# Performance work log

Hardware: AMD Instinct MI355X
Metric: run time of the kernel (lower is better)

Reference implementation:

```python
import jax, jax.numpy as jnp
import numpy as np

EPS = 1e-5
N_HEAD = 16


def layernorm(x, g, b):
    mu = jnp.mean(x, axis=-1, keepdims=True)
    var = jnp.mean(jnp.square(x - mu), axis=-1, keepdims=True)
    return (x - mu) * jax.lax.rsqrt(var + EPS) * g + b


def setup_inputs() -> dict:
    key = jax.random.key(0)
    ks = jax.random.split(key, 8)
    B, S, D = 4, 2048, 1024
    F = 4 * D
    s = 0.02
    return {
        "h": jax.random.normal(ks[0], (B, S, D), jnp.float32),
        "ln1_g": jnp.ones((D,), jnp.float32),
        "ln1_b": jnp.zeros((D,), jnp.float32),
        "wq": jax.random.normal(ks[1], (D, D), jnp.float32) * s,
        "bq": jnp.zeros((D,), jnp.float32),
        "wk": jax.random.normal(ks[2], (D, D), jnp.float32) * s,
        "bk": jnp.zeros((D,), jnp.float32),
        "wv": jax.random.normal(ks[3], (D, D), jnp.float32) * s,
        "bv": jnp.zeros((D,), jnp.float32),
        "wo": jax.random.normal(ks[4], (D, D), jnp.float32) * s,
        "bo": jnp.zeros((D,), jnp.float32),
        "ln2_g": jnp.ones((D,), jnp.float32),
        "ln2_b": jnp.zeros((D,), jnp.float32),
        "wfc": jax.random.normal(ks[5], (F, D), jnp.float32) * s,
        "bfc": jnp.zeros((F,), jnp.float32),
        "wproj": jax.random.normal(ks[6], (D, F), jnp.float32) * s,
        "bproj": jnp.zeros((D,), jnp.float32),
    }


def reference(h, ln1_g, ln1_b, wq, bq, wk, bk, wv, bv, wo, bo,
              ln2_g, ln2_b, wfc, bfc, wproj, bproj):
    B, S, D = h.shape
    H = N_HEAD
    Dh = D // H

    # --- attention sub-block ---
    r = h
    x = layernorm(h, ln1_g, ln1_b)
    q = (x @ wq.T + bq).reshape(B, S, H, Dh)
    k = (x @ wk.T + bk).reshape(B, S, H, Dh)
    v = (x @ wv.T + bv).reshape(B, S, H, Dh)

    scores = jnp.einsum("bqhd,bkhd->bhqk", q, k) / jnp.sqrt(jnp.float32(Dh))
    causal = jnp.tril(jnp.ones((S, S), bool))  # [S,S]
    scores = jnp.where(causal, scores, jnp.finfo(scores.dtype).min)
    probs = jax.nn.softmax(scores, axis=-1)
    o = jnp.einsum("bhqk,bkhd->bqhd", probs, v).reshape(B, S, D)
    h = r + (o @ wo.T + bo)

    # --- MLP sub-block ---
    r = h
    x = layernorm(h, ln2_g, ln2_b)
    x = jax.nn.gelu(x @ wfc.T + bfc, approximate=True)  # NewGELU (tanh)
    h = r + (x @ wproj.T + bproj)
    return h
```

## Files before the change

### kernel.cpp

```cpp
#include <hip/hip_runtime.h>
#include <hip/hip_bf16.h>
#include <stdint.h>


typedef short bf16x8 __attribute__((ext_vector_type(8)));
typedef float f32x4  __attribute__((ext_vector_type(4)));
typedef float f32x16 __attribute__((ext_vector_type(16)));
typedef short s16x4  __attribute__((ext_vector_type(4)));

__device__ __forceinline__ short f2bf(float f) {
  union { float f; uint32_t u; } a;
  a.f = f;
  uint32_t r = a.u + 0x7fffu + ((a.u >> 16) & 1u);
  return (short)(r >> 16);
}

__device__ __forceinline__ unsigned cvt_pk_bf16(float lo, float hi_) {
  unsigned r;
  asm("v_cvt_pk_bf16_f32 %0, %1, %2" : "=v"(r) : "v"(lo), "v"(hi_));
  return r;
}

__device__ __forceinline__ void gload_lds16(const void* g, void* l) {
  __builtin_amdgcn_global_load_lds(
      (const __attribute__((address_space(1))) void*)g,
      (__attribute__((address_space(3))) void*)l, 16, 0, 0);
}

__device__ __forceinline__ float gelu_f(float x) {
  float y = 0.7978845608028654f * (x + 0.044715f * x * x * x);
  y = fminf(fmaxf(y, -20.f), 20.f);
  float e = __expf(2.f * y);
  return 0.5f * x * (1.f + (e - 1.f) / (e + 1.f));
}

struct W6 {
  const float* s[6];
  short* d[6];
  int off[7];
};

__global__ __launch_bounds__(256)
void cvt_all(W6 a) {
  const int i = blockIdx.x * 256 + threadIdx.x;
#pragma unroll
  for (int k = 0; k < 6; ++k) {
    if (i >= a.off[k] && i < a.off[k + 1]) {
      const int j = i - a.off[k];
      float4 v = ((const float4*)a.s[k])[j];
      s16x4 o;
      o[0] = f2bf(v.x); o[1] = f2bf(v.y); o[2] = f2bf(v.z); o[3] = f2bf(v.w);
      ((s16x4*)a.d[k])[j] = o;
    }
  }
}

__global__ __launch_bounds__(256)
void ln_fwd(const float* __restrict__ x, const float* __restrict__ g,
            const float* __restrict__ b, short* __restrict__ y) {
  const long row = blockIdx.x;
  const int t = threadIdx.x;
  const float4 xv = ((const float4*)(x + row * 1024))[t];
  float s  = xv.x + xv.y + xv.z + xv.w;
  float ss = xv.x * xv.x + xv.y * xv.y + xv.z * xv.z + xv.w * xv.w;
#pragma unroll
  for (int m = 1; m < 64; m <<= 1) {
    s  += __shfl_xor(s, m);
    ss += __shfl_xor(ss, m);
  }
  __shared__ float rs[4], rss[4];
  const int wid = t >> 6, lane = t & 63;
  if (lane == 0) { rs[wid] = s; rss[wid] = ss; }
  __syncthreads();
  s  = rs[0] + rs[1] + rs[2] + rs[3];
  ss = rss[0] + rss[1] + rss[2] + rss[3];
  const float mu   = s * (1.f / 1024.f);
  const float var  = ss * (1.f / 1024.f) - mu * mu;
  const float rstd = rsqrtf(var + 1e-5f);
  const float4 gv = ((const float4*)g)[t];
  const float4 bv = ((const float4*)b)[t];
  s16x4 ov;
  ov[0] = f2bf((xv.x - mu) * rstd * gv.x + bv.x);
  ov[1] = f2bf((xv.y - mu) * rstd * gv.y + bv.y);
  ov[2] = f2bf((xv.z - mu) * rstd * gv.z + bv.z);
  ov[3] = f2bf((xv.w - mu) * rstd * gv.w + bv.w);
  *(s16x4*)(y + row * 1024 + t * 4) = ov;
}

template <int OUT_BF16, int HAS_RES, int HAS_GELU>
__global__ __launch_bounds__(256, 2)
void gemm_bt5(const short* __restrict__ A, const short* __restrict__ W,
              const float* __restrict__ bias, const float* __restrict__ res,
              void* __restrict__ out, int M, int N, int K) {
  __shared__ short As[128 * 64];
  __shared__ short Bs[256 * 64];
  const int tid = threadIdx.x;
  const int wid = tid >> 6, lane = tid & 63;
  const int l16 = lane & 15, lg = lane >> 4;
  const int wm = wid >> 1, wn = wid & 1;

  const int nbx = N >> 8;
  const int nwg = nbx * (M >> 7);
  int flat = (int)blockIdx.x;
  if ((nwg & 7) == 0) flat = (flat & 7) * (nwg >> 3) + (flat >> 3);
  const int brow = (flat / nbx) * 128, bcol = (flat % nbx) * 256;

  f32x4 acc[4][8] = {};

  const int r0 = tid >> 3, g0 = tid & 7;

  int ra[4], rb[8];
#pragma unroll
  for (int m = 0; m < 4; ++m) ra[m] = wm * 64 + m * 16 + l16;
#pragma unroll
  for (int n = 0; n < 8; ++n) rb[n] = wn * 128 + n * 16 + l16;

  for (int kt = 0; kt < K; kt += 64) {
    __syncthreads();
#pragma unroll
    for (int i = 0; i < 4; ++i) {
      const int row = i * 32 + r0;
      gload_lds16(A + (long)(brow + row) * K + kt + 8 * (g0 ^ (row & 7)),
                  &As[(i * 256 + tid) * 8]);
    }
#pragma unroll
    for (int i = 0; i < 8; ++i) {
      const int row = i * 32 + r0;
      gload_lds16(W + (long)(bcol + row) * K + kt + 8 * (g0 ^ (row & 7)),
                  &Bs[(i * 256 + tid) * 8]);
    }
    __syncthreads();

#pragma unroll
    for (int kk = 0; kk < 2; ++kk) {
      bf16x8 af[4], bf[8];
#pragma unroll
      for (int m = 0; m < 4; ++m)
        af[m] = *(const bf16x8*)&As[ra[m] * 64 + 8 * ((kk * 4 + lg) ^ (ra[m] & 7))];
#pragma unroll
      for (int n = 0; n < 8; ++n)
        bf[n] = *(const bf16x8*)&Bs[rb[n] * 64 + 8 * ((kk * 4 + lg) ^ (rb[n] & 7))];
#pragma unroll
      for (int m = 0; m < 4; ++m)
#pragma unroll
        for (int n = 0; n < 8; ++n)
          acc[m][n] = __builtin_amdgcn_mfma_f32_16x16x32_bf16(af[m], bf[n], acc[m][n], 0, 0, 0);
    }
  }

#pragma unroll
  for (int n = 0; n < 8; ++n) {
    const int col = bcol + wn * 128 + n * 16 + l16;
    const float bb = bias[col];
#pragma unroll
    for (int m = 0; m < 4; ++m) {
#pragma unroll
      for (int j = 0; j < 4; ++j) {
        const long row = brow + wm * 64 + m * 16 + lg * 4 + j;
        float vv = acc[m][n][j] + bb;
        if (HAS_GELU) vv = gelu_f(vv);
        if (HAS_RES) vv += res[row * N + col];
        if (OUT_BF16) ((short*)out)[row * N + col] = f2bf(vv);
        else          ((float*)out)[row * N + col] = vv;
      }
    }
  }
}

__global__ __launch_bounds__(256)
void transpose_v(const short* __restrict__ v, short* __restrict__ vtg,
                 int S, int ldv, int H) {
  __shared__ short t[64][66];
  const int bh = blockIdx.y, b = bh / H, hh = bh % H;
  const int s0 = blockIdx.x * 64;
  const int tid = threadIdx.x;
#pragma unroll
  for (int i = 0; i < 2; ++i) {
    const int c = i * 256 + tid;
    const int sl = c >> 3, d8 = (c & 7) * 8;
    bf16x8 vv = *(const bf16x8*)&v[((long)b * S + s0 + sl) * ldv + hh * 64 + d8];
#pragma unroll
    for (int j = 0; j < 8; ++j) t[d8 + j][sl] = vv[j];
  }
  __syncthreads();
#pragma unroll
  for (int i = 0; i < 2; ++i) {
    const int c = i * 256 + tid;
    const int dl = c >> 3, s8 = (c & 7) * 8;
    bf16x8 ov;
#pragma unroll
    for (int j = 0; j < 8; ++j) ov[j] = t[dl][s8 + j];
    *(bf16x8*)&vtg[((long)bh * 64 + dl) * S + s0 + s8] = ov;
  }
}

__global__ __launch_bounds__(256, 4)
void attn_fwd2(const short* __restrict__ qg, const short* __restrict__ kg,
               const short* __restrict__ vtg, short* __restrict__ og,
               int S, int ldq, int D, int H) {
  const int tid = threadIdx.x, wid = tid >> 6, lane = tid & 63;
  const int l31 = lane & 31, hi = lane >> 5;
  const int fid = blockIdx.x;
  const int bh = fid & 63;
  const int b = bh / H, hh = bh % H;
  static const int perm[16] = {15, 0, 8, 7, 1, 14, 6, 9, 13, 2, 10, 5, 3, 12, 4, 11};
  const int qt = perm[(fid >> 6) & 15];
  const int q0 = qt * 128;
  const long qbase = (long)b * S * ldq + hh * 64;
  const long obase = (long)b * S * D + hh * 64;
  const long vbase = (long)bh * 64 * S;

  __shared__ short Ks[2][64 * 64];
  __shared__ short Vs[2][64 * 64];

  auto STAGE = [&](int buf, int k0) {
#pragma unroll
    for (int i = 0; i < 2; ++i) {
      const int c = i * 256 + tid;
      const int row = c >> 3, gl = c & 7;
      gload_lds16(&kg[qbase + (long)(k0 + row) * ldq + 8 * (gl ^ (row & 7))],
                  &Ks[buf][(i * 256 + wid * 64) * 8]);
      gload_lds16(&vtg[vbase + (long)row * S + k0 + 8 * (gl ^ (row & 7))],
                  &Vs[buf][(i * 256 + wid * 64) * 8]);
    }
  };

  const float kScale = 0.125f * 1.44269504089f;

  const int qw = q0 + wid * 32;
  const int qv = qw + l31;

  bf16x8 qf[4];
#pragma unroll
  for (int s = 0; s < 4; ++s)
    qf[s] = *(const bf16x8*)&qg[qbase + (long)qv * ldq + 16 * s + 8 * hi];

  f32x16 oa[2] = {};
  float mr = -3000.f, lr = 0.f;

  const int ntiles = qt * 2 + 2;

  STAGE(0, 0);
  for (int t = 0; t < ntiles; ++t) {
    const int cur = t & 1;
    const int k0 = t * 64;
    if (t + 1 < ntiles) {
      STAGE(cur ^ 1, k0 + 64);
      asm volatile("s_waitcnt vmcnt(4)" ::: "memory");
    } else {
      asm volatile("s_waitcnt vmcnt(0)" ::: "memory");
    }
    __builtin_amdgcn_s_barrier();

    if (k0 < qw + 32) {
      f32x16 st[2] = {};
#pragma unroll
      for (int s = 0; s < 4; ++s) {
        const int g = ((s << 1) | hi) ^ (l31 & 7);
        bf16x8 kf0 = *(const bf16x8*)&Ks[cur][l31 * 64 + 8 * g];
        bf16x8 kf1 = *(const bf16x8*)&Ks[cur][(32 + l31) * 64 + 8 * g];
        st[0] = __builtin_amdgcn_mfma_f32_32x32x16_bf16(kf0, qf[s], st[0], 0, 0, 0);
        st[1] = __builtin_amdgcn_mfma_f32_32x32x16_bf16(kf1, qf[s], st[1], 0, 0, 0);
      }

      const bool need_mask = (k0 + 63 > qw);
      float pv[2][16];
#pragma unroll
      for (int kb = 0; kb < 2; ++kb)
#pragma unroll
        for (int r = 0; r < 16; ++r) {
          float v = st[kb][r] * kScale;
          if (need_mask) {
            const int key = k0 + kb * 32 + (r & 3) + 8 * (r >> 2) + 4 * hi;
            if (key > qv) v = -1e30f;
          }
          pv[kb][r] = v;
        }

      float t8[8];
#pragma unroll
      for (int j = 0; j < 8; ++j)
        t8[j] = fmaxf(fmaxf(pv[0][j], pv[0][8 + j]), fmaxf(pv[1][j], pv[1][8 + j]));
      float rm = fmaxf(fmaxf(fmaxf(t8[0], t8[1]), fmaxf(t8[2], t8[3])),
                       fmaxf(fmaxf(t8[4], t8[5]), fmaxf(t8[6], t8[7])));
      rm = fmaxf(rm, __shfl_xor(rm, 32));

      const bool defer = (bool)__all(rm <= mr + 8.f);
      const float mn = defer ? mr : fmaxf(mr, rm);

      float a0 = 0.f, a1 = 0.f, a2 = 0.f, a3 = 0.f;
#pragma unroll
      for (int r = 0; r < 8; ++r) {
        float p0 = exp2f(pv[0][r] - mn);      pv[0][r] = p0;      a0 += p0;
        float p1 = exp2f(pv[0][8 + r] - mn);  pv[0][8 + r] = p1;  a1 += p1;
        float p2 = exp2f(pv[1][r] - mn);      pv[1][r] = p2;      a2 += p2;
        float p3 = exp2f(pv[1][8 + r] - mn);  pv[1][8 + r] = p3;  a3 += p3;
      }
      float ls = (a0 + a1) + (a2 + a3);
      ls += __shfl_xor(ls, 32);

      if (!defer) {
        const float alpha = exp2f(mr - mn);
        lr = lr * alpha + ls;
        mr = mn;
#pragma unroll
        for (int r = 0; r < 16; ++r) {
          const int crow = (r & 3) + 8 * (r >> 2) + 4 * hi;
          const float ar = __shfl(alpha, crow | (lane & 32));
          oa[0][r] *= ar;
          oa[1][r] *= ar;
        }
      } else {
        lr += ls;
      }

      bf16x8 pa[4];
#pragma unroll
      for (int kb = 0; kb < 2; ++kb) {
        unsigned pk[8], ex[8];
#pragma unroll
        for (int i2 = 0; i2 < 8; ++i2)
          pk[i2] = cvt_pk_bf16(pv[kb][2 * i2], pv[kb][2 * i2 + 1]);
#pragma unroll
        for (int i2 = 0; i2 < 8; ++i2)
          ex[i2] = (unsigned)__shfl_xor((int)pk[i2], 32);
        union { unsigned u[4]; bf16x8 v8; } f0, f1;
        f0.u[0] = hi ? ex[2] : pk[0];
        f0.u[1] = hi ? ex[3] : pk[1];
        f0.u[2] = hi ? pk[2] : ex[0];
        f0.u[3] = hi ? pk[3] : ex[1];
        f1.u[0] = hi ? ex[6] : pk[4];
        f1.u[1] = hi ? ex[7] : pk[5];
        f1.u[2] = hi ? pk[6] : ex[4];
        f1.u[3] = hi ? pk[7] : ex[5];
        pa[2 * kb]     = f0.v8;
        pa[2 * kb + 1] = f1.v8;
      }

#pragma unroll
      for (int s = 0; s < 4; ++s) {
        const int g = ((s << 1) | hi) ^ (l31 & 7);
        bf16x8 vf0 = *(const bf16x8*)&Vs[cur][l31 * 64 + 8 * g];
        bf16x8 vf1 = *(const bf16x8*)&Vs[cur][(32 + l31) * 64 + 8 * g];
        oa[0] = __builtin_amdgcn_mfma_f32_32x32x16_bf16(pa[s], vf0, oa[0], 0, 0, 0);
        oa[1] = __builtin_amdgcn_mfma_f32_32x32x16_bf16(pa[s], vf1, oa[1], 0, 0, 0);
      }
    }

    asm volatile("s_waitcnt lgkmcnt(0)" ::: "memory");
    __builtin_amdgcn_s_barrier();
  }

  const float linv = 1.f / lr;
#pragma unroll
  for (int r = 0; r < 16; ++r) {
    const int crow = (r & 3) + 8 * (r >> 2) + 4 * hi;
    const float li = __shfl(linv, crow | (lane & 32));
    const long row = qw + crow;
    og[obase + row * D + l31]      = f2bf(oa[0][r] * li);
    og[obase + row * D + 32 + l31] = f2bf(oa[1][r] * li);
  }
}

extern "C" void kernel_launch(void* const* d_in, const int* in_sizes, int n_in,
                              void* d_out, int out_size, void* d_ws, size_t ws_size,
                              hipStream_t stream) {
  (void)in_sizes; (void)n_in; (void)out_size; (void)ws_size;
  const float* h     = (const float*)d_in[0];
  const float* ln1_g = (const float*)d_in[1];
  const float* ln1_b = (const float*)d_in[2];
  const float* wq    = (const float*)d_in[3];
  const float* bq    = (const float*)d_in[4];
  const float* wk    = (const float*)d_in[5];
  const float* bk    = (const float*)d_in[6];
  const float* wv    = (const float*)d_in[7];
  const float* bv    = (const float*)d_in[8];
  const float* wo    = (const float*)d_in[9];
  const float* bo    = (const float*)d_in[10];
  const float* ln2_g = (const float*)d_in[11];
  const float* ln2_b = (const float*)d_in[12];
  const float* wfc   = (const float*)d_in[13];
  const float* bfc   = (const float*)d_in[14];
  const float* wproj = (const float*)d_in[15];
  const float* bproj = (const float*)d_in[16];

  const int B = 4, S = 2048, D = 1024, H = 16, F = 4096, T = B * S;
  const int D3 = 3 * D;

  char* ws = (char*)d_ws;
  size_t off = 0;
  auto alloc = [&](size_t bytes) {
    void* p = ws + off;
    off += (bytes + 255) & ~(size_t)255;
    return p;
  };
  short* xb   = (short*)alloc((size_t)T * D * 2);
  short* qkv  = (short*)alloc((size_t)T * D3 * 2);
  short* ob   = (short*)alloc((size_t)T * D * 2);
  float* h2   = (float*)alloc((size_t)T * D * 4);
  short* wqkvb  = (short*)alloc((size_t)D3 * D * 2);
  short* wob    = (short*)alloc((size_t)D * D * 2);
  short* wfcb   = (short*)alloc((size_t)F * D * 2);
  short* wprojb = (short*)alloc((size_t)D * F * 2);
  float* bqkv   = (float*)alloc((size_t)D3 * 4);
  short* ub  = qkv;
  short* vtg = (short*)h2;

  W6 wargs;
  const int nqq = D * D / 4;
  wargs.s[0] = wq;    wargs.d[0] = wqkvb;
  wargs.s[1] = wk;    wargs.d[1] = wqkvb + (size_t)D * D;
  wargs.s[2] = wv;    wargs.d[2] = wqkvb + (size_t)2 * D * D;
  wargs.s[3] = wo;    wargs.d[3] = wob;
  wargs.s[4] = wfc;   wargs.d[4] = wfcb;
  wargs.s[5] = wproj; wargs.d[5] = wprojb;
  wargs.off[0] = 0;
  wargs.off[1] = nqq;
  wargs.off[2] = 2 * nqq;
  wargs.off[3] = 3 * nqq;
  wargs.off[4] = 4 * nqq;
  wargs.off[5] = 4 * nqq + F * D / 4;
  wargs.off[6] = 4 * nqq + 2 * (F * D / 4);
  cvt_all<<<dim3(wargs.off[6] / 256), 256, 0, stream>>>(wargs);
  hipMemcpyAsync(bqkv,         bq, D * 4, hipMemcpyDeviceToDevice, stream);
  hipMemcpyAsync(bqkv + D,     bk, D * 4, hipMemcpyDeviceToDevice, stream);
  hipMemcpyAsync(bqkv + 2 * D, bv, D * 4, hipMemcpyDeviceToDevice, stream);

  ln_fwd<<<dim3(T), 256, 0, stream>>>(h, ln1_g, ln1_b, xb);
  gemm_bt5<1, 0, 0><<<dim3((T / 128) * (D3 / 256)), 256, 0, stream>>>(
      xb, wqkvb, bqkv, nullptr, qkv, T, D3, D);
  transpose_v<<<dim3(S / 64, B * H), 256, 0, stream>>>(qkv + 2 * D, vtg, S, D3, H);
  attn_fwd2<<<dim3((S / 128) * (B * H / 64) * 64), 256, 0, stream>>>(
      qkv, qkv + D, vtg, ob, S, D3, D, H);
  gemm_bt5<0, 1, 0><<<dim3((T / 128) * (D / 256)), 256, 0, stream>>>(
      ob, wob, bo, h, h2, T, D, D);

  ln_fwd<<<dim3(T), 256, 0, stream>>>(h2, ln2_g, ln2_b, xb);
  gemm_bt5<1, 0, 1><<<dim3((T / 128) * (F / 256)), 256, 0, stream>>>(
      xb, wfcb, bfc, nullptr, ub, T, F, D);
  gemm_bt5<0, 1, 0><<<dim3((T / 128) * (D / 256)), 256, 0, stream>>>(
      ub, wprojb, bproj, h2, (float*)d_out, T, D, F);
}
```

Baseline: 402.8 us.

## Fold softmax scale into Q projection and use 128x128 tiles for N=1024 GEMMs

The softmax scale (1/sqrt(Dh)·log2e) is now applied in the QKV GEMM epilogue to the Q columns, so the attention kernel no longer multiplies every score by the scale. A new gemm_bt6 with 128x128 tiles replaces the 128x256 tiles for the two N=1024 output GEMMs (Wo and Wproj), doubling the workgroup count to improve CU occupancy on those smaller problems. The row-max reduction in attention is restructured into chained three-input max operations. Scaling Q before the bf16 rounding slightly changes numerics, and smaller tiles reduce per-block data reuse.

```diff
diff --git a/kernel.cpp b/kernel.cpp
--- a/kernel.cpp
+++ b/kernel.cpp
@@ -19,6 +19,10 @@
   unsigned r;
   asm("v_cvt_pk_bf16_f32 %0, %1, %2" : "=v"(r) : "v"(lo), "v"(hi_));
   return r;
+}
+
+__device__ __forceinline__ float m3(float a, float b, float c) {
+  return fmaxf(fmaxf(a, b), c);
 }
 
 __device__ __forceinline__ void gload_lds16(const void* g, void* l) {
@@ -87,7 +91,7 @@
   *(s16x4*)(y + row * 1024 + t * 4) = ov;
 }
 
-template <int OUT_BF16, int HAS_RES, int HAS_GELU>
+template <int OUT_BF16, int HAS_RES, int HAS_GELU, int SCALE_Q>
 __global__ __launch_bounds__(256, 2)
 void gemm_bt5(const short* __restrict__ A, const short* __restrict__ W,
               const float* __restrict__ bias, const float* __restrict__ res,
@@ -151,6 +155,84 @@
 #pragma unroll
   for (int n = 0; n < 8; ++n) {
     const int col = bcol + wn * 128 + n * 16 + l16;
+    const float bb = bias[col];
+    const bool doScale = SCALE_Q && (col < N / 3);
+#pragma unroll
+    for (int m = 0; m < 4; ++m) {
+#pragma unroll
+      for (int j = 0; j < 4; ++j) {
+        const long row = brow + wm * 64 + m * 16 + lg * 4 + j;
+        float vv = acc[m][n][j] + bb;
+        if (HAS_GELU) vv = gelu_f(vv);
+        if (HAS_RES) vv += res[row * N + col];
+        if (SCALE_Q && doScale) vv *= 0.18033688f;
+        if (OUT_BF16) ((short*)out)[row * N + col] = f2bf(vv);
+        else          ((float*)out)[row * N + col] = vv;
+      }
+    }
+  }
+}
+
+template <int OUT_BF16, int HAS_RES, int HAS_GELU>
+__global__ __launch_bounds__(256, 2)
+void gemm_bt6(const short* __restrict__ A, const short* __restrict__ W,
+              const float* __restrict__ bias, const float* __restrict__ res,
+              void* __restrict__ out, int M, int N, int K) {
+  __shared__ short As[128 * 64];
+  __shared__ short Bs[128 * 64];
+  const int tid = threadIdx.x;
+  const int wid = tid >> 6, lane = tid & 63;
+  const int l16 = lane & 15, lg = lane >> 4;
+  const int wm = wid >> 1, wn = wid & 1;
+
+  const int nbx = N >> 7;
+  const int nwg = nbx * (M >> 7);
+  int flat = (int)blockIdx.x;
+  if ((nwg & 7) == 0) flat = (flat & 7) * (nwg >> 3) + (flat >> 3);
+  const int brow = (flat / nbx) * 128, bcol = (flat % nbx) * 128;
+
+  f32x4 acc[4][4] = {};
+
+  const int r0 = tid >> 3, g0 = tid & 7;
+
+  int ra[4], rb[4];
+#pragma unroll
+  for (int m = 0; m < 4; ++m) ra[m] = wm * 64 + m * 16 + l16;
+#pragma unroll
+  for (int n = 0; n < 4; ++n) rb[n] = wn * 64 + n * 16 + l16;
+
+  for (int kt = 0; kt < K; kt += 64) {
+    __syncthreads();
+#pragma unroll
+    for (int i = 0; i < 4; ++i) {
+      const int row = i * 32 + r0;
+      gload_lds16(A + (long)(brow + row) * K + kt + 8 * (g0 ^ (row & 7)),
+                  &As[(i * 256 + tid) * 8]);
+      gload_lds16(W + (long)(bcol + row) * K + kt + 8 * (g0 ^ (row & 7)),
+                  &Bs[(i * 256 + tid) * 8]);
+    }
+    __syncthreads();
+
+#pragma unroll
+    for (int kk = 0; kk < 2; ++kk) {
+      bf16x8 af[4], bf[4];
+#pragma unroll
+      for (int m = 0; m < 4; ++m)
+        af[m] = *(const bf16x8*)&As[ra[m] * 64 + 8 * ((kk * 4 + lg) ^ (ra[m] & 7))];
+#pragma unroll
+      for (int n = 0; n < 4; ++n)
+        bf[n] = *(const bf16x8*)&Bs[rb[n] * 64 + 8 * ((kk * 4 + lg) ^ (rb[n] & 7))];
+#pragma unroll
+      for (int m = 0; m < 4; ++m)
+#pragma unroll
+        for (int n = 0; n < 4; ++n)
+          acc[m][n] = __builtin_amdgcn_mfma_f32_16x16x32_bf16(af[m], bf[n], acc[m][n], 0, 0, 0);
+    }
+  }
+
+#pragma unroll
+  for (int n = 0; n < 4; ++n) {
+    const int col = bcol + wn * 64 + n * 16 + l16;
     const float bb = bias[col];
 #pragma unroll
     for (int m = 0; m < 4; ++m) {
@@ -225,8 +307,6 @@
     }
   };
 
-  const float kScale = 0.125f * 1.44269504089f;
-
   const int qw = q0 + wid * 32;
   const int qv = qw + l31;
 
@@ -269,7 +349,7 @@
       for (int kb = 0; kb < 2; ++kb)
 #pragma unroll
         for (int r = 0; r < 16; ++r) {
-          float v = st[kb][r] * kScale;
+          float v = st[kb][r];
           if (need_mask) {
             const int key = k0 + kb * 32 + (r & 3) + 8 * (r >> 2) + 4 * hi;
             if (key > qv) v = -1e30f;
@@ -277,12 +357,11 @@
           pv[kb][r] = v;
         }
 
-      float t8[8];
-#pragma unroll
-      for (int j = 0; j < 8; ++j)
-        t8[j] = fmaxf(fmaxf(pv[0][j], pv[0][8 + j]), fmaxf(pv[1][j], pv[1][8 + j]));
-      float rm = fmaxf(fmaxf(fmaxf(t8[0], t8[1]), fmaxf(t8[2], t8[3])),
-                       fmaxf(fmaxf(t8[4], t8[5]), fmaxf(t8[6], t8[7])));
+      float rm = fmaxf(pv[0][0], pv[0][1]);
+#pragma unroll
+      for (int r = 2; r < 16; r += 2) rm = m3(rm, pv[0][r], pv[0][r + 1]);
+#pragma unroll
+      for (int r = 0; r < 16; r += 2) rm = m3(rm, pv[1][r], pv[1][r + 1]);
       rm = fmaxf(rm, __shfl_xor(rm, 32));
 
       const bool defer = (bool)__all(rm <= mr + 8.f);
@@ -427,17 +506,17 @@
   hipMemcpyAsync(bqkv + 2 * D, bv, D * 4, hipMemcpyDeviceToDevice, stream);
 
   ln_fwd<<<dim3(T), 256, 0, stream>>>(h, ln1_g, ln1_b, xb);
-  gemm_bt5<1, 0, 0><<<dim3((T / 128) * (D3 / 256)), 256, 0, stream>>>(
+  gemm_bt5<1, 0, 0, 1><<<dim3((T / 128) * (D3 / 256)), 256, 0, stream>>>(
       xb, wqkvb, bqkv, nullptr, qkv, T, D3, D);
   transpose_v<<<dim3(S / 64, B * H), 256, 0, stream>>>(qkv + 2 * D, vtg, S, D3, H);
   attn_fwd2<<<dim3((S / 128) * (B * H / 64) * 64), 256, 0, stream>>>(
       qkv, qkv + D, vtg, ob, S, D3, D, H);
-  gemm_bt5<0, 1, 0><<<dim3((T / 128) * (D / 256)), 256, 0, stream>>>(
+  gemm_bt6<0, 1, 0><<<dim3((T / 128) * (D / 128)), 256, 0, stream>>>(
       ob, wob, bo, h, h2, T, D, D);
 
   ln_fwd<<<dim3(T), 256, 0, stream>>>(h2, ln2_g, ln2_b, xb);
-  gemm_bt5<1, 0, 1><<<dim3((T / 128) * (F / 256)), 256, 0, stream>>>(
+  gemm_bt5<1, 0, 1, 0><<<dim3((T / 128) * (F / 256)), 256, 0, stream>>>(
       xb, wfcb, bfc, nullptr, ub, T, F, D);
-  gemm_bt5<0, 1, 0><<<dim3((T / 128) * (D / 256)), 256, 0, stream>>>(
+  gemm_bt6<0, 1, 0><<<dim3((T / 128) * (D / 128)), 256, 0, stream>>>(
       ub, wprojb, bproj, h2, (float*)d_out, T, D, F);
 }
```

New measurement: 384.2 us. -4.6%, faster.
